# Optimization experiments

Hardware: AMD Instinct MI355X
Metric: run time of the kernel (lower is better)

## Reference

```python
import jax, jax.numpy as jnp
import numpy as np

EMBED = 1024
HEADS = 16
HEAD_DIM = EMBED // HEADS


def setup_inputs() -> dict:
    key = jax.random.key(0)
    ks = jax.random.split(key, 7)
    N, S, E = 4, 2048, EMBED
    s = 1.0 / np.sqrt(E)
    return {
        "values_in": jax.random.normal(ks[0], (N, S, E), jnp.float32),
        "keys_in": jax.random.normal(ks[1], (N, S, E), jnp.float32),
        "query_in": jax.random.normal(ks[2], (N, S, E), jnp.float32),
        # nn.Linear(E, E, bias=False): y = x @ W.T; store W as [out, in]
        "W_v": jax.random.normal(ks[3], (E, E), jnp.float32) * s,
        "W_k": jax.random.normal(ks[4], (E, E), jnp.float32) * s,
        "W_q": jax.random.normal(ks[5], (E, E), jnp.float32) * s,
        "W_o": jax.random.normal(ks[6], (E, E), jnp.float32) * s,
    }


def reference(values_in, keys_in, query_in, W_v, W_k, W_q, W_o):
    N, Sq, E = query_in.shape
    H, D = HEADS, HEAD_DIM
    v = (values_in @ W_v.T).reshape(N, -1, H, D)
    k = (keys_in @ W_k.T).reshape(N, -1, H, D)
    q = (query_in @ W_q.T).reshape(N, Sq, H, D)
    # scores scaled by sqrt(embed_size), faithful to source (not sqrt(head_dim))
    energy = jnp.einsum("nqhd,nkhd->nhqk", q, k) / jnp.sqrt(jnp.float32(E)).astype(q.dtype)
    attn = jax.nn.softmax(energy, axis=-1)
    out = jnp.einsum("nhqk,nkhd->nqhd", attn, v).reshape(N, Sq, E)
    return out @ W_o.T
```

## Files before the change

### kernel.cpp

```cpp
#include <hip/hip_runtime.h>
#include <hip/hip_bf16.h>
#include <stdint.h>

typedef __bf16 bf16_t;
typedef __bf16 bf16x8 __attribute__((ext_vector_type(8)));
typedef __bf16 bf16x4 __attribute__((ext_vector_type(4)));
typedef float  f32x4  __attribute__((ext_vector_type(4)));

#define GL_LDS16(g, l)                                                         \
  __builtin_amdgcn_global_load_lds(                                            \
      (const __attribute__((address_space(1))) void*)(g),                      \
      (__attribute__((address_space(3))) void*)(l), 16, 0, 0)

#define MFMA16 __builtin_amdgcn_mfma_f32_16x16x32_bf16

#define SC2 0.04508422f

__global__ void cvt_w_kernel(const float* __restrict__ s0, const float* __restrict__ s1,
                             const float* __restrict__ s2, const float* __restrict__ s3,
                             bf16_t* __restrict__ dst) {
  const int b = blockIdx.x;
  const float* src = (b < 1024) ? s0 : (b < 2048) ? s1 : (b < 3072) ? s2 : s3;
  const int i = ((b & 1023) * 256 + threadIdx.x) * 4;
  f32x4 v = *(const f32x4*)(src + i);
  bf16x4 w;
  w[0] = (bf16_t)v[0]; w[1] = (bf16_t)v[1]; w[2] = (bf16_t)v[2]; w[3] = (bf16_t)v[3];
  *(bf16x4*)(dst + (size_t)(b >> 10) * (1u << 20) + i) = w;
}

__global__ __launch_bounds__(256) void proj_kernel(const float* __restrict__ Aq,
                                                   const float* __restrict__ Ak,
                                                   const float* __restrict__ Av,
                                                   const bf16_t* __restrict__ Wbase,
                                                   bf16_t* __restrict__ Oq,
                                                   bf16_t* __restrict__ Ok,
                                                   bf16_t* __restrict__ Ovt) {
  __shared__ char ldsA[128 * 64 * 2];
  __shared__ char ldsB[128 * 64 * 2];
  const int z  = blockIdx.z;
  const float* Af = (z == 0) ? Aq : (z == 1) ? Ak : Av;
  const bf16_t* Wptr = Wbase + ((size_t)z << 20);
  const int t  = threadIdx.x;
  const int l  = t & 63;
  const int wv = t >> 6;
  const int wr = wv >> 1, wc = wv & 1;
  const int lq = l & 15, lg = l >> 4;
  const int bid = blockIdx.x + (blockIdx.y << 6);
  const int pm  = (bid & 7) * 64 + (bid >> 3);
  const int m0  = (pm >> 3) * 128;
  const int n0  = (pm & 7) * 128;

  const int ar = t >> 4;
  const int ac = (t & 15) * 4;

  f32x4 acc[4][4] = {};

  for (int k0 = 0; k0 < 1024; k0 += 64) {
#pragma unroll
    for (int it = 0; it < 4; ++it) {
      const int dst = it * 4096 + t * 16;
      const int row = dst >> 7;
      const int col = (dst & 127) >> 1;
      GL_LDS16(Wptr + (size_t)(n0 + row) * 1024 + k0 + col, ldsB + dst);
    }
#pragma unroll
    for (int u = 0; u < 8; ++u) {
      const int row = u * 16 + ar;
      f32x4 v = *(const f32x4*)(Af + (size_t)(m0 + row) * 1024 + k0 + ac);
      bf16x4 b;
      b[0] = (bf16_t)v[0]; b[1] = (bf16_t)v[1]; b[2] = (bf16_t)v[2]; b[3] = (bf16_t)v[3];
      *(bf16x4*)(ldsA + row * 128 + ac * 2) = b;
    }
    __syncthreads();
#pragma unroll
    for (int kc = 0; kc < 2; ++kc) {
      bf16x8 af[4], bfr[4];
#pragma unroll
      for (int mm = 0; mm < 4; ++mm)
        af[mm] = *(const bf16x8*)(ldsA + (wr * 64 + mm * 16 + lq) * 128 + kc * 64 + lg * 16);
#pragma unroll
      for (int nn = 0; nn < 4; ++nn)
        bfr[nn] = *(const bf16x8*)(ldsB + (wc * 64 + nn * 16 + lq) * 128 + kc * 64 + lg * 16);
#pragma unroll
      for (int mm = 0; mm < 4; ++mm)
#pragma unroll
        for (int nn = 0; nn < 4; ++nn)
          acc[mm][nn] = MFMA16(af[mm], bfr[nn], acc[mm][nn], 0, 0, 0);
    }
    __syncthreads();
  }

  if (z == 2) {
#pragma unroll
    for (int mm = 0; mm < 4; ++mm)
#pragma unroll
      for (int nn = 0; nn < 4; ++nn) {
        const int r  = m0 + wr * 64 + mm * 16 + lg * 4;
        const int c  = n0 + wc * 64 + nn * 16 + lq;
        const int nb = r >> 11, s = r & 2047;
        const int hh = c >> 6, d = c & 63;
        bf16x4 w;
#pragma unroll
        for (int i = 0; i < 4; ++i) w[i] = (bf16_t)acc[mm][nn][i];
        *(bf16x4*)(Ovt + (((size_t)nb * 16 + hh) * 64 + d) * 2048 + s) = w;
      }
  } else {
    bf16_t* O      = (z == 0) ? Oq : Ok;
    const float sc = (z == 0) ? SC2 : 1.0f;
#pragma unroll
    for (int mm = 0; mm < 4; ++mm)
#pragma unroll
      for (int nn = 0; nn < 4; ++nn) {
#pragma unroll
        for (int i = 0; i < 4; ++i) {
          const int r  = m0 + wr * 64 + mm * 16 + lg * 4 + i;
          const int c  = n0 + wc * 64 + nn * 16 + lq;
          const int nb = r >> 11, s = r & 2047;
          const int hh = c >> 6, d = c & 63;
          O[(((size_t)nb * 16 + hh) * 2048 + s) * 64 + d] = (bf16_t)(acc[mm][nn][i] * sc);
        }
      }
  }
}

__global__ __launch_bounds__(256) void ogemm_kernel(const bf16_t* __restrict__ Ab,
                                                    const bf16_t* __restrict__ Wptr,
                                                    float* __restrict__ O) {
  __shared__ char ldsA[128 * 64 * 2];
  __shared__ char ldsB[128 * 64 * 2];
  const int t  = threadIdx.x;
  const int l  = t & 63;
  const int wv = t >> 6;
  const int wr = wv >> 1, wc = wv & 1;
  const int lq = l & 15, lg = l >> 4;
  const int bid = blockIdx.x + (blockIdx.y << 6);
  const int pm  = (bid & 7) * 64 + (bid >> 3);
  const int m0  = (pm >> 3) * 128;
  const int n0  = (pm & 7) * 128;

  f32x4 acc[4][4] = {};

  for (int k0 = 0; k0 < 1024; k0 += 64) {
#pragma unroll
    for (int it = 0; it < 4; ++it) {
      const int dst = it * 4096 + t * 16;
      const int row = dst >> 7;
      const int col = (dst & 127) >> 1;
      GL_LDS16(Wptr + (size_t)(n0 + row) * 1024 + k0 + col, ldsB + dst);
      GL_LDS16(Ab + (size_t)(m0 + row) * 1024 + k0 + col, ldsA + dst);
    }
    __syncthreads();
#pragma unroll
    for (int kc = 0; kc < 2; ++kc) {
      bf16x8 af[4], bfr[4];
#pragma unroll
      for (int mm = 0; mm < 4; ++mm)
        af[mm] = *(const bf16x8*)(ldsA + (wr * 64 + mm * 16 + lq) * 128 + kc * 64 + lg * 16);
#pragma unroll
      for (int nn = 0; nn < 4; ++nn)
        bfr[nn] = *(const bf16x8*)(ldsB + (wc * 64 + nn * 16 + lq) * 128 + kc * 64 + lg * 16);
#pragma unroll
      for (int mm = 0; mm < 4; ++mm)
#pragma unroll
        for (int nn = 0; nn < 4; ++nn)
          acc[mm][nn] = MFMA16(af[mm], bfr[nn], acc[mm][nn], 0, 0, 0);
    }
    __syncthreads();
  }
#pragma unroll
  for (int mm = 0; mm < 4; ++mm)
#pragma unroll
    for (int nn = 0; nn < 4; ++nn) {
      const int r = m0 + wr * 64 + mm * 16 + lg * 4;
      const int c = n0 + wc * 64 + nn * 16 + lq;
#pragma unroll
      for (int i = 0; i < 4; ++i) O[(size_t)(r + i) * 1024 + c] = acc[mm][nn][i];
    }
}

__device__ __forceinline__ void sm_pv(const f32x4& s0v, const f32x4& s1v, float& mrun,
                                      float& lsum, const bf16x8 vf[4], f32x4 o[4]) {
  float s[8];
#pragma unroll
  for (int i = 0; i < 4; ++i) { s[i] = s0v[i]; s[4 + i] = s1v[i]; }
  float tm = fmaxf(fmaxf(fmaxf(s[0], s[1]), fmaxf(s[2], s[3])),
                   fmaxf(fmaxf(s[4], s[5]), fmaxf(s[6], s[7])));
  if (__any(tm > mrun + 8.f)) {
    tm = fmaxf(tm, __shfl_xor(tm, 16));
    tm = fmaxf(tm, __shfl_xor(tm, 32));
    const float mnew = fmaxf(mrun, tm);
    const float corr = exp2f(mrun - mnew);
    lsum *= corr;
#pragma unroll
    for (int c = 0; c < 4; ++c)
#pragma unroll
      for (int i = 0; i < 4; ++i) o[c][i] *= corr;
    mrun = mnew;
  }
  float p[8], ps = 0.f;
#pragma unroll
  for (int j = 0; j < 8; ++j) { p[j] = exp2f(s[j] - mrun); ps += p[j]; }
  lsum += ps;
  bf16x8 pf;
#pragma unroll
  for (int j = 0; j < 8; ++j) pf[j] = (bf16_t)p[j];
  __builtin_amdgcn_s_setprio(1);
#pragma unroll
  for (int c = 0; c < 4; ++c) o[c] = MFMA16(vf[c], pf, o[c], 0, 0, 0);
  __builtin_amdgcn_s_setprio(0);
}

__global__ __launch_bounds__(256, 4) void attn_kernel(const bf16_t* __restrict__ Q,
                                                      const bf16_t* __restrict__ K,
                                                      const bf16_t* __restrict__ Vt,
                                                      bf16_t* __restrict__ AO) {
  __shared__ char ldsc[32768];
  const int t  = threadIdx.x;
  const int l  = t & 63;
  const int wv = t >> 6;
  const int lq = l & 15, lg = l >> 4;
  const int bid  = blockIdx.x;
  const int flat = (bid & 7) * 128 + (bid >> 3);
  const int qb = flat & 15, h = (flat >> 4) & 15, n = flat >> 8;
  const int s0 = qb * 128 + wv * 32;
  const size_t hoff = ((size_t)(n * 16 + h)) * 2048 * 64;
  const bf16_t* Qb  = Q + hoff;
  const bf16_t* Kb  = K + hoff;
  const bf16_t* Vtb = Vt + hoff;

  const bf16x8 qx0 = *(const bf16x8*)(Qb + (s0 + lq) * 64 + lg * 8);
  const bf16x8 qx1 = *(const bf16x8*)(Qb + (s0 + lq) * 64 + 32 + lg * 8);
  const bf16x8 qy0 = *(const bf16x8*)(Qb + (s0 + 16 + lq) * 64 + lg * 8);
  const bf16x8 qy1 = *(const bf16x8*)(Qb + (s0 + 16 + lq) * 64 + 32 + lg * 8);

  f32x4 ox[4] = {}, oy[4] = {};
  float mx = -1e30f, lx = 0.f, my = -1e30f, ly = 0.f;

  const int g1      = t >> 6;
  const int lqt     = t & 15;
  const int lgt     = (t >> 4) & 3;
  const int kperm_t = 8 * (lqt >> 2) + (lqt & 3);
  const int krow0   = (g1 >> 1) * 4 + kperm_t;
  const int kcol0   = (g1 & 1) * 32 + lgt * 8;
  const int vrow0   = 16 * g1 + lqt;
  const int vcol0   = lgt * 8;

#define STAGE(bofs, kt)                                                           \
  {                                                                               \
    const int kv0_ = (kt) * 64;                                                   \
    GL_LDS16(Kb + (size_t)(kv0_ + krow0) * 64 + kcol0, ldsc + (bofs) + t * 16);   \
    GL_LDS16(Kb + (size_t)(kv0_ + krow0 + 32) * 64 + kcol0,                       \
             ldsc + (bofs) + 4096 + t * 16);                                      \
    GL_LDS16(Vtb + (size_t)vrow0 * 2048 + kv0_ + vcol0,                           \
             ldsc + (bofs) + 8192 + t * 16);                                      \
    GL_LDS16(Vtb + (size_t)vrow0 * 2048 + kv0_ + vcol0 + 32,                      \
             ldsc + (bofs) + 12288 + t * 16);                                     \
  }
#define WAITV4 asm volatile("s_waitcnt vmcnt(4)" ::: "memory")
#define WAITV0 asm volatile("s_waitcnt vmcnt(0)" ::: "memory")
#define BARRIER                                                                   \
  __builtin_amdgcn_s_barrier();                                                   \
  __builtin_amdgcn_sched_barrier(0)
#define STEP(PB)                                                                  \
  {                                                                               \
    const char* kp_ = (const char*)ldsc + (PB) + l * 16;                          \
    const bf16x8 kf0 = *(const bf16x8*)(kp_);                                     \
    const bf16x8 kf1 = *(const bf16x8*)(kp_ + 1024);                              \
    const bf16x8 kf2 = *(const bf16x8*)(kp_ + 2048);                              \
    const bf16x8 kf3 = *(const bf16x8*)(kp_ + 3072);                              \
    bf16x8 vfr[4];                                                                \
    vfr[0] = *(const bf16x8*)(kp_ + 8192);                                        \
    vfr[1] = *(const bf16x8*)(kp_ + 9216);                                        \
    vfr[2] = *(const bf16x8*)(kp_ + 10240);                                       \
    vfr[3] = *(const bf16x8*)(kp_ + 11264);                                       \
    f32x4 zz = {};                                                                \
    __builtin_amdgcn_s_setprio(1);                                                \
    f32x4 sX0 = MFMA16(kf0, qx0, zz, 0, 0, 0);                                    \
    sX0 = MFMA16(kf1, qx1, sX0, 0, 0, 0);                                         \
    f32x4 sX1 = MFMA16(kf2, qx0, zz, 0, 0, 0);                                    \
    sX1 = MFMA16(kf3, qx1, sX1, 0, 0, 0);                                         \
    f32x4 sY0 = MFMA16(kf0, qy0, zz, 0, 0, 0);                                    \
    sY0 = MFMA16(kf1, qy1, sY0, 0, 0, 0);                                         \
    f32x4 sY1 = MFMA16(kf2, qy0, zz, 0, 0, 0);                                    \
    sY1 = MFMA16(kf3, qy1, sY1, 0, 0, 0);                                         \
    __builtin_amdgcn_s_setprio(0);                                                \
    sm_pv(sX0, sX1, mx, lx, vfr, ox);                                             \
    sm_pv(sY0, sY1, my, ly, vfr, oy);                                             \
  }

  STAGE(0, 0);
  for (int kt = 0; kt < 32; kt += 2) {
    STAGE(16384, kt + 1);
    WAITV4;
    BARRIER;
    STEP(0);
    STEP(4096);
    BARRIER;
    if (kt + 2 < 32) {
      STAGE(0, kt + 2);
      WAITV4;
    } else {
      WAITV0;
    }
    BARRIER;
    STEP(16384);
    STEP(16384 + 4096);
    BARRIER;
  }
#undef STAGE
#undef WAITV4
#undef WAITV0
#undef BARRIER
#undef STEP

  lx += __shfl_xor(lx, 16); lx += __shfl_xor(lx, 32);
  ly += __shfl_xor(ly, 16); ly += __shfl_xor(ly, 32);
  const float invx = 1.f / lx;
  const float invy = 1.f / ly;
  bf16_t* AOx = AO + (((size_t)(n * 2048 + s0 + lq)) * 16 + h) * 64 + lg * 4;
  bf16_t* AOy = AO + (((size_t)(n * 2048 + s0 + 16 + lq)) * 16 + h) * 64 + lg * 4;
#pragma unroll
  for (int c = 0; c < 4; ++c) {
    bf16x4 w;
#pragma unroll
    for (int i = 0; i < 4; ++i) w[i] = (bf16_t)(ox[c][i] * invx);
    *(bf16x4*)(AOx + c * 16) = w;
#pragma unroll
    for (int i = 0; i < 4; ++i) w[i] = (bf16_t)(oy[c][i] * invy);
    *(bf16x4*)(AOy + c * 16) = w;
  }
}

extern "C" void kernel_launch(void* const* d_in, const int* in_sizes, int n_in,
                              void* d_out, int out_size, void* d_ws, size_t ws_size,
                              hipStream_t stream) {
  const float* values = (const float*)d_in[0];
  const float* keys   = (const float*)d_in[1];
  const float* query  = (const float*)d_in[2];
  const float* Wv     = (const float*)d_in[3];
  const float* Wk     = (const float*)d_in[4];
  const float* Wq     = (const float*)d_in[5];
  const float* Wo     = (const float*)d_in[6];
  float* out          = (float*)d_out;

  char* ws     = (char*)d_ws;
  bf16_t* w_b  = (bf16_t*)ws;
  bf16_t* wo_b = w_b + (3u << 20);
  bf16_t* q_b  = w_b + (4u << 20);
  bf16_t* k_b  = q_b + (8u << 20);
  bf16_t* vt_b = k_b + (8u << 20);
  bf16_t* ao_b = vt_b + (8u << 20);

  cvt_w_kernel<<<4096, 256, 0, stream>>>(Wq, Wk, Wv, Wo, w_b);

  proj_kernel<<<dim3(64, 8, 3), 256, 0, stream>>>(query, keys, values, w_b, q_b, k_b, vt_b);

  attn_kernel<<<1024, 256, 0, stream>>>(q_b, k_b, vt_b, ao_b);

  ogemm_kernel<<<dim3(64, 8), 256, 0, stream>>>(ao_b, wo_b, out);
}
```

Measured before the change: 376.1 us.

## Double-buffer and XOR-swizzle LDS tiles in projection and output GEMMs

Both GEMM kernels now keep two LDS buffers and issue the next k-tile's global-to-LDS loads, plus register prefetch of the fp32 activations in the projection kernel, before computing on the current tile. Explicit vmcnt waits and raw barriers replace __syncthreads. The LDS layout also gains an XOR swizzle on the 16-byte column chunk to reduce bank conflicts on the MFMA fragment reads. In exchange, LDS use doubles to 64KB per block and register pressure rises from the 16 prefetched f32x4 values, which may lower occupancy.

```diff
diff --git a/kernel.cpp b/kernel.cpp
--- a/kernel.cpp
+++ b/kernel.cpp
@@ -13,6 +13,12 @@
       (__attribute__((address_space(3))) void*)(l), 16, 0, 0)
 
 #define MFMA16 __builtin_amdgcn_mfma_f32_16x16x32_bf16
+
+#define WAITVM(N) asm volatile("s_waitcnt vmcnt(" #N ")" ::: "memory")
+#define WAITLGKM asm volatile("s_waitcnt lgkmcnt(0)" ::: "memory")
+#define BARRIER                                                                \
+  __builtin_amdgcn_s_barrier();                                                \
+  __builtin_amdgcn_sched_barrier(0)
 
 #define SC2 0.04508422f
 
@@ -35,8 +41,8 @@
                                                    bf16_t* __restrict__ Oq,
                                                    bf16_t* __restrict__ Ok,
                                                    bf16_t* __restrict__ Ovt) {
-  __shared__ char ldsA[128 * 64 * 2];
-  __shared__ char ldsB[128 * 64 * 2];
+  __shared__ char ldsA[2][16384];
+  __shared__ char ldsB[2][16384];
   const int z  = blockIdx.z;
   const float* Af = (z == 0) ? Aq : (z == 1) ? Ak : Av;
   const bf16_t* Wptr = Wbase + ((size_t)z << 20);
@@ -50,45 +56,72 @@
   const int m0  = (pm >> 3) * 128;
   const int n0  = (pm & 7) * 128;
 
-  const int ar = t >> 4;
-  const int ac = (t & 15) * 4;
+  const int ar    = t >> 4;
+  const int ac    = (t & 15) * 4;
+  const int abyte = (t & 15) * 8;
+  const int awz   = (ar & 7) << 4;
+  const int wrow  = t >> 3;
+  const int wcolb = ((t & 7) * 16) ^ (((t >> 3) & 7) << 4);
+  const int rxor  = (lq & 7) << 4;
 
   f32x4 acc[4][4] = {};
-
-  for (int k0 = 0; k0 < 1024; k0 += 64) {
-#pragma unroll
-    for (int it = 0; it < 4; ++it) {
-      const int dst = it * 4096 + t * 16;
-      const int row = dst >> 7;
-      const int col = (dst & 127) >> 1;
-      GL_LDS16(Wptr + (size_t)(n0 + row) * 1024 + k0 + col, ldsB + dst);
+  f32x4 ra[8], rb[8];
+
+#define LOADA(regs, kt)                                                         \
+  { _Pragma("unroll") for (int u = 0; u < 8; ++u)                               \
+      regs[u] = *(const f32x4*)(Af + (size_t)(m0 + u * 16 + ar) * 1024 +        \
+                                (kt) * 64 + ac); }
+#define STAGEW(buf, kt)                                                         \
+  { _Pragma("unroll") for (int it = 0; it < 4; ++it) {                          \
+      const int row_ = it * 32 + wrow;                                          \
+      GL_LDS16(Wptr + (size_t)(n0 + row_) * 1024 + (kt) * 64 + (wcolb >> 1),    \
+               ldsB[buf] + it * 4096 + t * 16); } }
+#define WRITEA(buf, regs)                                                       \
+  { _Pragma("unroll") for (int u = 0; u < 8; ++u) {                             \
+      bf16x4 b_;                                                                \
+      b_[0] = (bf16_t)regs[u][0]; b_[1] = (bf16_t)regs[u][1];                   \
+      b_[2] = (bf16_t)regs[u][2]; b_[3] = (bf16_t)regs[u][3];                   \
+      *(bf16x4*)(ldsA[buf] + (u * 16 + ar) * 128 + (abyte ^ awz)) = b_; } }
+#define GCOMPUTE(buf)                                                           \
+  { _Pragma("unroll") for (int kc = 0; kc < 2; ++kc) {                          \
+      bf16x8 af[4], bfr[4];                                                     \
+      _Pragma("unroll") for (int mm = 0; mm < 4; ++mm)                          \
+        af[mm] = *(const bf16x8*)(ldsA[buf] + (wr * 64 + mm * 16 + lq) * 128 +  \
+                                  ((kc * 64 + lg * 16) ^ rxor));                \
+      _Pragma("unroll") for (int nn = 0; nn < 4; ++nn)                          \
+        bfr[nn] = *(const bf16x8*)(ldsB[buf] + (wc * 64 + nn * 16 + lq) * 128 + \
+                                   ((kc * 64 + lg * 16) ^ rxor));               \
+      _Pragma("unroll") for (int mm = 0; mm < 4; ++mm)                          \
+        _Pragma("unroll") for (int nn = 0; nn < 4; ++nn)                        \
+          acc[mm][nn] = MFMA16(af[mm], bfr[nn], acc[mm][nn], 0, 0, 0); } }
+
+  LOADA(ra, 0);
+  STAGEW(0, 0);
+  for (int kt = 0; kt < 16; kt += 2) {
+    LOADA(rb, kt + 1);
+    STAGEW(1, kt + 1);
+    WAITVM(12);
+    WRITEA(0, ra);
+    WAITLGKM;
+    BARRIER;
+    GCOMPUTE(0);
+    BARRIER;
+    if (kt < 14) {
+      LOADA(ra, kt + 2);
+      STAGEW(0, kt + 2);
+      WAITVM(12);
+    } else {
+      WAITVM(0);
     }
-#pragma unroll
-    for (int u = 0; u < 8; ++u) {
-      const int row = u * 16 + ar;
-      f32x4 v = *(const f32x4*)(Af + (size_t)(m0 + row) * 1024 + k0 + ac);
-      bf16x4 b;
-      b[0] = (bf16_t)v[0]; b[1] = (bf16_t)v[1]; b[2] = (bf16_t)v[2]; b[3] = (bf16_t)v[3];
-      *(bf16x4*)(ldsA + row * 128 + ac * 2) = b;
-    }
-    __syncthreads();
-#pragma unroll
-    for (int kc = 0; kc < 2; ++kc) {
-      bf16x8 af[4], bfr[4];
-#pragma unroll
-      for (int mm = 0; mm < 4; ++mm)
-        af[mm] = *(const bf16x8*)(ldsA + (wr * 64 + mm * 16 + lq) * 128 + kc * 64 + lg * 16);
-#pragma unroll
-      for (int nn = 0; nn < 4; ++nn)
-        bfr[nn] = *(const bf16x8*)(ldsB + (wc * 64 + nn * 16 + lq) * 128 + kc * 64 + lg * 16);
-#pragma unroll
-      for (int mm = 0; mm < 4; ++mm)
-#pragma unroll
-        for (int nn = 0; nn < 4; ++nn)
-          acc[mm][nn] = MFMA16(af[mm], bfr[nn], acc[mm][nn], 0, 0, 0);
-    }
-    __syncthreads();
-  }
+    WRITEA(1, rb);
+    WAITLGKM;
+    BARRIER;
+    GCOMPUTE(1);
+    BARRIER;
+  }
+#undef LOADA
+#undef STAGEW
+#undef WRITEA
 
   if (z == 2) {
 #pragma unroll
@@ -126,8 +159,8 @@
 __global__ __launch_bounds__(256) void ogemm_kernel(const bf16_t* __restrict__ Ab,
                                                     const bf16_t* __restrict__ Wptr,
                                                     float* __restrict__ O) {
-  __shared__ char ldsA[128 * 64 * 2];
-  __shared__ char ldsB[128 * 64 * 2];
+  __shared__ char ldsA[2][16384];
+  __shared__ char ldsB[2][16384];
   const int t  = threadIdx.x;
   const int l  = t & 63;
   const int wv = t >> 6;
@@ -138,35 +171,40 @@
   const int m0  = (pm >> 3) * 128;
   const int n0  = (pm & 7) * 128;
 
+  const int wrow  = t >> 3;
+  const int wcolb = ((t & 7) * 16) ^ (((t >> 3) & 7) << 4);
+  const int rxor  = (lq & 7) << 4;
+
   f32x4 acc[4][4] = {};
 
-  for (int k0 = 0; k0 < 1024; k0 += 64) {
-#pragma unroll
-    for (int it = 0; it < 4; ++it) {
-      const int dst = it * 4096 + t * 16;
-      const int row = dst >> 7;
-      const int col = (dst & 127) >> 1;
-      GL_LDS16(Wptr + (size_t)(n0 + row) * 1024 + k0 + col, ldsB + dst);
-      GL_LDS16(Ab + (size_t)(m0 + row) * 1024 + k0 + col, ldsA + dst);
+#define STAGEAB(buf, kt)                                                        \
+  { _Pragma("unroll") for (int it = 0; it < 4; ++it) {                          \
+      const int row_ = it * 32 + wrow;                                          \
+      GL_LDS16(Ab + (size_t)(m0 + row_) * 1024 + (kt) * 64 + (wcolb >> 1),      \
+               ldsA[buf] + it * 4096 + t * 16);                                 \
+      GL_LDS16(Wptr + (size_t)(n0 + row_) * 1024 + (kt) * 64 + (wcolb >> 1),    \
+               ldsB[buf] + it * 4096 + t * 16); } }
+
+  STAGEAB(0, 0);
+  for (int kt = 0; kt < 16; kt += 2) {
+    STAGEAB(1, kt + 1);
+    WAITVM(8);
+    BARRIER;
+    GCOMPUTE(0);
+    BARRIER;
+    if (kt < 14) {
+      STAGEAB(0, kt + 2);
+      WAITVM(8);
+    } else {
+      WAITVM(0);
     }
-    __syncthreads();
-#pragma unroll
-    for (int kc = 0; kc < 2; ++kc) {
-      bf16x8 af[4], bfr[4];
-#pragma unroll
-      for (int mm = 0; mm < 4; ++mm)
-        af[mm] = *(const bf16x8*)(ldsA + (wr * 64 + mm * 16 + lq) * 128 + kc * 64 + lg * 16);
-#pragma unroll
-      for (int nn = 0; nn < 4; ++nn)
-        bfr[nn] = *(const bf16x8*)(ldsB + (wc * 64 + nn * 16 + lq) * 128 + kc * 64 + lg * 16);
-#pragma unroll
-      for (int mm = 0; mm < 4; ++mm)
-#pragma unroll
-        for (int nn = 0; nn < 4; ++nn)
-          acc[mm][nn] = MFMA16(af[mm], bfr[nn], acc[mm][nn], 0, 0, 0);
-    }
-    __syncthreads();
-  }
+    BARRIER;
+    GCOMPUTE(1);
+    BARRIER;
+  }
+#undef STAGEAB
+#undef GCOMPUTE
+
 #pragma unroll
   for (int mm = 0; mm < 4; ++mm)
 #pragma unroll
@@ -256,11 +294,6 @@
     GL_LDS16(Vtb + (size_t)vrow0 * 2048 + kv0_ + vcol0 + 32,                      \
              ldsc + (bofs) + 12288 + t * 16);                                     \
   }
-#define WAITV4 asm volatile("s_waitcnt vmcnt(4)" ::: "memory")
-#define WAITV0 asm volatile("s_waitcnt vmcnt(0)" ::: "memory")
-#define BARRIER                                                                   \
-  __builtin_amdgcn_s_barrier();                                                   \
-  __builtin_amdgcn_sched_barrier(0)
 #define STEP(PB)                                                                  \
   {                                                                               \
     const char* kp_ = (const char*)ldsc + (PB) + l * 16;                          \
@@ -291,16 +324,16 @@
   STAGE(0, 0);
   for (int kt = 0; kt < 32; kt += 2) {
     STAGE(16384, kt + 1);
-    WAITV4;
+    WAITVM(4);
     BARRIER;
     STEP(0);
     STEP(4096);
     BARRIER;
     if (kt + 2 < 32) {
       STAGE(0, kt + 2);
-      WAITV4;
+      WAITVM(4);
     } else {
-      WAITV0;
+      WAITVM(0);
     }
     BARRIER;
     STEP(16384);
@@ -308,9 +341,6 @@
     BARRIER;
   }
 #undef STAGE
-#undef WAITV4
-#undef WAITV0
-#undef BARRIER
 #undef STEP
 
   lx += __shfl_xor(lx, 16); lx += __shfl_xor(lx, 32);
```

Result: slower. 412.5 us (+9.7%).
